# Kernel optimization log

Measured on AMD Instinct MI355X. Metric: run time of the kernel, lower is better.

## Reference

```python
import jax, jax.numpy as jnp
import numpy as np

HIDDEN = 2048
N_HEADS = 16
HEAD_DIM = HIDDEN // N_HEADS
MAX_POS = 4096
ROPE_THETA = 10000.0
B, S = 2, 4096


def rotate_half(x):
    d = x.shape[-1] // 2
    return jnp.concatenate([-x[..., d:], x[..., :d]], axis=-1)


def make_rope_cache(seq_len, dim, base):
    inv_freq = 1.0 / (base ** (np.arange(0, dim, 2, dtype=np.float32) / dim))
    t = np.arange(seq_len, dtype=np.float32)
    freqs = np.einsum('i,j->ij', t, inv_freq)
    emb = np.concatenate([freqs, freqs], axis=-1)
    return jnp.asarray(np.cos(emb)), jnp.asarray(np.sin(emb))


def setup_inputs() -> dict:
    key = jax.random.key(0)
    k1, k2, k3, k4, k5, k6 = jax.random.split(key, 6)
    hidden_states = jax.random.normal(k1, (B, S, HIDDEN), dtype=jnp.float32)
    # causal additive mask [B,1,S,S]
    causal = jnp.where(jnp.tril(jnp.ones((S, S), dtype=bool)), 0.0, -1e9).astype(jnp.float32)
    attention_mask = jnp.broadcast_to(causal[None, None], (B, 1, S, S))
    position_ids = jnp.broadcast_to(jnp.arange(S, dtype=jnp.int64)[None], (B, S))
    scale = 0.02
    Wq = jax.random.normal(k2, (HIDDEN, HIDDEN), dtype=jnp.float32) * scale
    Wk = jax.random.normal(k3, (HIDDEN, HIDDEN), dtype=jnp.float32) * scale
    Wv = jax.random.normal(k4, (HIDDEN, HIDDEN), dtype=jnp.float32) * scale
    Wo = jax.random.normal(k5, (HIDDEN, HIDDEN), dtype=jnp.float32) * scale
    return {"hidden_states": hidden_states, "attention_mask": attention_mask,
            "position_ids": position_ids, "Wq": Wq, "Wk": Wk, "Wv": Wv, "Wo": Wo}


def reference(hidden_states, attention_mask, position_ids, Wq, Wk, Wv, Wo):
    bsz, q_len, _ = hidden_states.shape
    # projections (torch Linear: x @ W.T; here W stored as [in,out] -> x @ W)
    q = (hidden_states @ Wq).reshape(bsz, q_len, N_HEADS, HEAD_DIM).transpose(0, 2, 1, 3)
    k = (hidden_states @ Wk).reshape(bsz, q_len, N_HEADS, HEAD_DIM).transpose(0, 2, 1, 3)
    v = (hidden_states @ Wv).reshape(bsz, q_len, N_HEADS, HEAD_DIM).transpose(0, 2, 1, 3)
    cos_c, sin_c = make_rope_cache(q_len, HEAD_DIM, ROPE_THETA)
    cos = cos_c[position_ids][:, None]  # [B,1,S,Dh]
    sin = sin_c[position_ids][:, None]
    q = q * cos + rotate_half(q) * sin
    k = k * cos + rotate_half(k) * sin
    scores = jnp.einsum('bhqd,bhkd->bhqk', q, k) / jnp.sqrt(jnp.float32(HEAD_DIM))
    scores = scores + attention_mask
    probs = jax.nn.softmax(scores.astype(jnp.float32), axis=-1).astype(q.dtype)
    attn = jnp.einsum('bhqk,bhkd->bhqd', probs, v)
    attn = attn.transpose(0, 2, 1, 3).reshape(bsz, q_len, HIDDEN)
    return attn @ Wo
```

## Files before the change

kernel.cpp:

```cpp
#include <hip/hip_runtime.h>

#define HID 2048
#define NHEADS 16
#define DHEAD 128
#define BB 2
#define SS 4096
#define MTOT (BB * SS)

typedef __attribute__((ext_vector_type(8))) short short8;
typedef __attribute__((ext_vector_type(8))) unsigned short ushort8;
typedef __attribute__((ext_vector_type(4))) float floatx4;
typedef __attribute__((ext_vector_type(16))) float floatx16;

static __device__ __forceinline__ ushort f2bf(float f) {
  unsigned x = __float_as_uint(f);
  return (ushort)((x + 0x7fffu + ((x >> 16) & 1u)) >> 16);
}
static __device__ __forceinline__ float bf2f(ushort u) {
  return __uint_as_float(((unsigned)u) << 16);
}
static __device__ __forceinline__ unsigned cvtpk_bf16(float lo, float hi) {
  unsigned r;
  asm("v_cvt_pk_bf16_f32 %0, %1, %2" : "=v"(r) : "v"(lo), "v"(hi));
  return r;
}
static __device__ __forceinline__ void pl32swap(unsigned& a, unsigned& b) {
  asm volatile("v_permlane32_swap_b32 %0, %1" : "+v"(a), "+v"(b));
}
static __device__ __forceinline__ float exp2_fast(float x) {
  float r;
  asm("v_exp_f32 %0, %1" : "=v"(r) : "v"(x));
  return r;
}
static __device__ __forceinline__ floatx16 fz16() {
  floatx16 z;
#pragma unroll
  for (int i = 0; i < 16; i++) z[i] = 0.f;
  return z;
}

#define GL16(g, l)                                                   \
  __builtin_amdgcn_global_load_lds(                                  \
      (const __attribute__((address_space(1))) unsigned int*)(g),    \
      (__attribute__((address_space(3))) unsigned int*)(l), 16, 0, 0)

__global__ __launch_bounds__(256) void k_prep(const float* __restrict__ X,
                                              ushort* __restrict__ Xb,
                                              const float* __restrict__ Wq,
                                              const float* __restrict__ Wk,
                                              const float* __restrict__ Wv,
                                              const float* __restrict__ Wo,
                                              ushort* __restrict__ Wqt,
                                              ushort* __restrict__ Wkt,
                                              ushort* __restrict__ Wvt,
                                              ushort* __restrict__ Wot,
                                              float* __restrict__ cosT,
                                              float* __restrict__ sinT) {
  __shared__ float tile[64][65];
  int id = blockIdx.x, t = threadIdx.x;
  if (id < 2048) {
    int i = id * 256 + t;
    const int n4 = MTOT * HID / 4, stride = 2048 * 256;
    for (; i < n4; i += stride) {
      float4 v = reinterpret_cast<const float4*>(X)[i];
      ushort4 u;
      u.x = f2bf(v.x); u.y = f2bf(v.y); u.z = f2bf(v.z); u.w = f2bf(v.w);
      reinterpret_cast<ushort4*>(Xb)[i] = u;
    }
  } else if (id < 6144) {
    int w = (id - 2048) >> 10;
    int bid = (id - 2048) & 1023;
    const float* W = (w == 0) ? Wq : (w == 1) ? Wk : (w == 2) ? Wv : Wo;
    ushort* Wt = (w == 0) ? Wqt : (w == 1) ? Wkt : (w == 2) ? Wvt : Wot;
    int n0 = (bid & 31) * 64, k0 = (bid >> 5) * 64;
#pragma unroll
    for (int i = 0; i < 16; i++) {
      int idx = t + i * 256, r = idx >> 6, c = idx & 63;
      tile[r][c] = W[(size_t)(k0 + r) * HID + n0 + c];
    }
    __syncthreads();
#pragma unroll
    for (int i = 0; i < 16; i++) {
      int idx = t + i * 256, r = idx >> 6, c = idx & 63;
      Wt[(size_t)(n0 + r) * HID + k0 + c] = f2bf(tile[c][r]);
    }
  } else {
    int idx = (id - 6144) * 256 + t;
    int pos = idx >> 6, j = idx & 63;
    float inv = powf(10000.0f, -(float)(2 * j) * (1.0f / 128.0f));
    float a = (float)pos * inv;
    cosT[idx] = cosf(a);
    sinT[idx] = sinf(a);
  }
}

__global__ __launch_bounds__(512) void k_rope(ushort* __restrict__ Q,
                                              ushort* __restrict__ Kb,
                                              const float* __restrict__ cosT,
                                              const float* __restrict__ sinT) {
  const float kSc = 0.12751742f;
  int idx = blockIdx.x * 512 + threadIdx.x;
  int j8 = (idx & 7) * 8;
  int hh = (idx >> 3) & (NHEADS - 1);
  int srow = idx >> 7;
  int pos = srow & (SS - 1);
  float4 c0 = *reinterpret_cast<const float4*>(&cosT[pos * 64 + j8]);
  float4 c1 = *reinterpret_cast<const float4*>(&cosT[pos * 64 + j8 + 4]);
  float4 s0 = *reinterpret_cast<const float4*>(&sinT[pos * 64 + j8]);
  float4 s1 = *reinterpret_cast<const float4*>(&sinT[pos * 64 + j8 + 4]);
  float cc[8] = {c0.x, c0.y, c0.z, c0.w, c1.x, c1.y, c1.z, c1.w};
  float ss[8] = {s0.x, s0.y, s0.z, s0.w, s1.x, s1.y, s1.z, s1.w};
  size_t base = (size_t)srow * HID + hh * DHEAD + j8;
  ushort8 qa = *reinterpret_cast<ushort8*>(&Q[base]);
  ushort8 qb = *reinterpret_cast<ushort8*>(&Q[base + 64]);
  ushort8 ka = *reinterpret_cast<ushort8*>(&Kb[base]);
  ushort8 kb = *reinterpret_cast<ushort8*>(&Kb[base + 64]);
  ushort8 o1, o2, o3, o4;
#pragma unroll
  for (int i = 0; i < 8; i++) {
    float a1 = bf2f(qa[i]), a2 = bf2f(qb[i]);
    o1[i] = f2bf((a1 * cc[i] - a2 * ss[i]) * kSc);
    o2[i] = f2bf((a2 * cc[i] + a1 * ss[i]) * kSc);
    float b1 = bf2f(ka[i]), b2 = bf2f(kb[i]);
    o3[i] = f2bf(b1 * cc[i] - b2 * ss[i]);
    o4[i] = f2bf(b2 * cc[i] + b1 * ss[i]);
  }
  *reinterpret_cast<ushort8*>(&Q[base]) = o1;
  *reinterpret_cast<ushort8*>(&Q[base + 64]) = o2;
  *reinterpret_cast<ushort8*>(&Kb[base]) = o3;
  *reinterpret_cast<ushort8*>(&Kb[base + 64]) = o4;
}

template <int OUT_BF16, int TRIPLE>
__global__ __launch_bounds__(512, 2) void k_gemm8(const ushort* __restrict__ A,
                                                  const ushort* __restrict__ Bt,
                                                  void* __restrict__ Cp,
                                                  const ushort* __restrict__ Bt2,
                                                  void* __restrict__ Cp2,
                                                  const ushort* __restrict__ A3,
                                                  const ushort* __restrict__ Bt3,
                                                  void* __restrict__ Cp3,
                                                  int Nc0, int Kd) {
  __shared__ ushort As[3][256 * 32];
  __shared__ ushort Bs[3][256 * 32];
  int t = threadIdx.x;
  int lane = t & 63, wid = t >> 6;
  int lrow = lane & 15, lk = lane >> 4;
  int wr = wid >> 2, wc = wid & 3;

  int id = blockIdx.x;
  int Nc = Nc0;
  if (TRIPLE && id >= 512) {
    A = A3; Bt = Bt3; Cp = Cp3; Nc = MTOT;
    id -= 512;
  } else if (TRIPLE && id >= 256) {
    Bt = Bt2; Cp = Cp2;
    id -= 256;
  }
  int nbx = Nc >> 8;
  int swz = (id & 7) * 32 + (id >> 3);
  int m0 = (swz / nbx) << 8, n0 = (swz % nbx) << 8;

  floatx4 acc[8][4];
#pragma unroll
  for (int i = 0; i < 8; i++)
#pragma unroll
    for (int j = 0; j < 4; j++) acc[i][j] = (floatx4){0.f, 0.f, 0.f, 0.f};

  int arow = t >> 2;
  int acol = (((t & 3) ^ (arow & 3)) << 3);
  const ushort* gA = A + (size_t)(m0 + arow) * Kd + acol;
  const ushort* gB = Bt + (size_t)(n0 + arow) * Kd + acol;

  auto STAGE = [&](int buf, int kt) {
    const ushort* a = gA + kt * 32;
    const ushort* bq = gB + kt * 32;
    GL16(a, (char*)As + buf * 16384 + t * 16);
    GL16(a + (size_t)128 * Kd, (char*)As + buf * 16384 + t * 16 + 8192);
    GL16(bq, (char*)Bs + buf * 16384 + t * 16);
    GL16(bq + (size_t)128 * Kd, (char*)Bs + buf * 16384 + t * 16 + 8192);
  };

  STAGE(0, 0);
  STAGE(1, 1);

  int nk = Kd >> 5;
  for (int tK = 0; tK < nk; ++tK) {
    if (tK + 1 < nk)
      asm volatile("s_waitcnt vmcnt(4)" ::: "memory");
    else
      asm volatile("s_waitcnt vmcnt(0)" ::: "memory");
    __builtin_amdgcn_s_barrier();
    asm volatile("" ::: "memory");
    int buf = tK % 3;
    const char* Ab_ = (const char*)As + buf * 16384;
    const char* Bb_ = (const char*)Bs + buf * 16384;
    short8 af[8], bfr[4];
#pragma unroll
    for (int fm = 0; fm < 8; fm++) {
      int row = wr * 128 + fm * 16 + lrow;
      af[fm] = *reinterpret_cast<const short8*>(
          Ab_ + ((row * 64 + lk * 16) ^ ((row & 3) << 4)));
    }
#pragma unroll
    for (int fn = 0; fn < 4; fn++) {
      int row = wc * 64 + fn * 16 + lrow;
      bfr[fn] = *reinterpret_cast<const short8*>(
          Bb_ + ((row * 64 + lk * 16) ^ ((row & 3) << 4)));
    }
    if (tK + 2 < nk) STAGE((tK + 2) % 3, tK + 2);
    __builtin_amdgcn_s_setprio(1);
#pragma unroll
    for (int fm = 0; fm < 8; fm++)
#pragma unroll
      for (int fn = 0; fn < 4; fn++)
        acc[fm][fn] = __builtin_amdgcn_mfma_f32_16x16x32_bf16(af[fm], bfr[fn],
                                                              acc[fm][fn], 0, 0, 0);
    __builtin_amdgcn_s_setprio(0);
  }

#pragma unroll
  for (int am = 0; am < 8; am++)
#pragma unroll
    for (int an = 0; an < 4; an++)
#pragma unroll
      for (int r = 0; r < 4; r++) {
        int m = m0 + wr * 128 + am * 16 + lk * 4 + r;
        int n = n0 + wc * 64 + an * 16 + lrow;
        if (OUT_BF16)
          ((ushort*)Cp)[(size_t)m * Nc + n] = f2bf(acc[am][an][r]);
        else
          ((float*)Cp)[(size_t)m * Nc + n] = acc[am][an][r];
      }
}

__global__ __launch_bounds__(512, 2) void k_fattn(const ushort* __restrict__ Qg,
                                                  const ushort* __restrict__ Kg,
                                                  const ushort* __restrict__ Vt2,
                                                  ushort* __restrict__ Og) {
  __shared__ ushort Ks[2][64 * 128];
  __shared__ ushort Vs[2][128 * 64];
  int t = threadIdx.x, lane = t & 63, wid = t >> 6;
  int l31 = lane & 31, hi = lane >> 5;
  int id = blockIdx.x;
  int qt = 15 - (id >> 5);
  int h = id & 15, b = (id >> 4) & 1;

  auto STAGE = [&](int buf, int kt) {
    int kv0 = kt * 64;
    const ushort* Kbase = Kg + (size_t)(b * SS + kv0) * HID + h * DHEAD;
    const ushort* Vbase = Vt2 + (size_t)(h * DHEAD) * MTOT + b * SS + kv0;
#pragma unroll
    for (int i = 0; i < 2; i++) {
      int L = t + i * 512;
      int row = L >> 4, cr = L & 15;
      GL16(Kbase + (size_t)row * HID + ((cr ^ (row & 15)) << 3),
           (char*)Ks + buf * 16384 + L * 16);
    }
#pragma unroll
    for (int i = 0; i < 2; i++) {
      int L = t + i * 512;
      int row = L >> 3, cr = L & 7;
      GL16(Vbase + (size_t)row * MTOT + ((cr ^ (row & 7)) << 3),
           (char*)Vs + buf * 16384 + L * 16);
    }
  };

  int q0 = qt * 256;
  int wq0 = q0 + wid * 32;
  int qlane = wq0 + l31;

  short8 qf[8];
  {
    const ushort* qb = Qg + (size_t)(b * SS + qlane) * HID + h * DHEAD + hi * 8;
#pragma unroll
    for (int ks = 0; ks < 8; ks++)
      qf[ks] = *reinterpret_cast<const short8*>(qb + ks * 16);
  }

  floatx16 accO[4];
#pragma unroll
  for (int db = 0; db < 4; db++) accO[db] = fz16();
  float mrow = -1e30f, lsum = 0.f;

  int nkt = (qt + 1) * 4;
  STAGE(0, 0);

  for (int kt = 0; kt < nkt; kt++) {
    int cur = kt & 1;
    int kv0 = kt * 64;
    bool pre = (kt + 1 < nkt);
    if (pre) {
      STAGE(cur ^ 1, kt + 1);
      asm volatile("s_waitcnt vmcnt(4)" ::: "memory");
    } else {
      asm volatile("s_waitcnt vmcnt(0)" ::: "memory");
    }
    __builtin_amdgcn_s_barrier();
    asm volatile("" ::: "memory");

    if (kv0 <= wq0 + 31) {
      const char* Kb_ = (const char*)Ks + cur * 16384;
      floatx16 accS[2];
      accS[0] = fz16(); accS[1] = fz16();
      __builtin_amdgcn_s_setprio(1);
#pragma unroll
      for (int ks = 0; ks < 8; ks++) {
#pragma unroll
        for (int kvb = 0; kvb < 2; kvb++) {
          int row = kvb * 32 + l31;
          int byte_ = (row * 256 + ks * 32 + hi * 16) ^ ((row & 15) << 4);
          short8 kf = *reinterpret_cast<const short8*>(Kb_ + byte_);
          accS[kvb] = __builtin_amdgcn_mfma_f32_32x32x16_bf16(kf, qf[ks], accS[kvb], 0, 0, 0);
        }
      }
      __builtin_amdgcn_s_setprio(0);

      if (kv0 + 63 > wq0) {
        int kvbase = kv0 + hi * 4;
#pragma unroll
        for (int kvb = 0; kvb < 2; kvb++)
#pragma unroll
          for (int r = 0; r < 16; r++) {
            int kvi = kvbase + kvb * 32 + (r & 3) + 8 * (r >> 2);
            if (kvi > qlane) accS[kvb][r] = -1e30f;
          }
      }

      float mA = -1e30f, mB = -1e30f, mC = -1e30f, mD = -1e30f;
#pragma unroll
      for (int r = 0; r < 16; r += 4) {
        mA = fmaxf(mA, fmaxf(accS[0][r], accS[1][r]));
        mB = fmaxf(mB, fmaxf(accS[0][r + 1], accS[1][r + 1]));
        mC = fmaxf(mC, fmaxf(accS[0][r + 2], accS[1][r + 2]));
        mD = fmaxf(mD, fmaxf(accS[0][r + 3], accS[1][r + 3]));
      }
      float mx = fmaxf(fmaxf(mA, mB), fmaxf(mC, mD));
      mx = fmaxf(mx, __shfl_xor(mx, 32));
      if (!__all(mx <= mrow + 8.0f)) {
        float mnew = fmaxf(mrow, mx);
        float corr = exp2_fast(mrow - mnew);
        mrow = mnew;
        lsum *= corr;
#pragma unroll
        for (int db = 0; db < 4; db++)
#pragma unroll
          for (int r = 0; r < 16; r++) accO[db][r] *= corr;
      }

      float sA = 0.f, sB = 0.f, sC = 0.f, sD = 0.f;
#pragma unroll
      for (int kvb = 0; kvb < 2; kvb++)
#pragma unroll
        for (int r = 0; r < 16; r += 4) {
          float p0 = exp2_fast(accS[kvb][r] - mrow);
          float p1 = exp2_fast(accS[kvb][r + 1] - mrow);
          float p2 = exp2_fast(accS[kvb][r + 2] - mrow);
          float p3 = exp2_fast(accS[kvb][r + 3] - mrow);
          accS[kvb][r] = p0; accS[kvb][r + 1] = p1;
          accS[kvb][r + 2] = p2; accS[kvb][r + 3] = p3;
          sA += p0; sB += p1; sC += p2; sD += p3;
        }
      lsum += ((sA + sB) + (sC + sD));

      const char* Vb_ = (const char*)Vs + cur * 16384;
#pragma unroll
      for (int ks = 0; ks < 4; ks++) {
        int kvb = ks >> 1, tt = ks & 1;
        unsigned w0 = cvtpk_bf16(accS[kvb][8 * tt + 0], accS[kvb][8 * tt + 1]);
        unsigned w2 = cvtpk_bf16(accS[kvb][8 * tt + 4], accS[kvb][8 * tt + 5]);
        pl32swap(w0, w2);
        unsigned w1 = cvtpk_bf16(accS[kvb][8 * tt + 2], accS[kvb][8 * tt + 3]);
        unsigned w3 = cvtpk_bf16(accS[kvb][8 * tt + 6], accS[kvb][8 * tt + 7]);
        pl32swap(w1, w3);
        union { unsigned u[4]; short8 v; } pf;
        pf.u[0] = w0; pf.u[1] = w1; pf.u[2] = w2; pf.u[3] = w3;
        __builtin_amdgcn_s_setprio(1);
#pragma unroll
        for (int db = 0; db < 4; db++) {
          int row = db * 32 + l31;
          int byte_ = (row * 128 + ks * 32 + hi * 16) ^ ((row & 7) << 4);
          short8 vf = *reinterpret_cast<const short8*>(Vb_ + byte_);
          accO[db] = __builtin_amdgcn_mfma_f32_32x32x16_bf16(vf, pf.v, accO[db], 0, 0, 0);
        }
        __builtin_amdgcn_s_setprio(0);
      }
    }
    asm volatile("" ::: "memory");
    __builtin_amdgcn_s_barrier();
    asm volatile("" ::: "memory");
  }

  float lt = lsum + __shfl_xor(lsum, 32);
  float inv = 1.0f / lt;
  char* sb = ((wid < 4) ? (char*)Ks : (char*)Vs) + (wid & 3) * 8192;
#pragma unroll
  for (int db = 0; db < 4; db++)
#pragma unroll
    for (int r = 0; r < 16; r += 2) {
      int d = db * 32 + (r & 3) + 8 * (r >> 2) + hi * 4;
      unsigned w = cvtpk_bf16(accO[db][r] * inv, accO[db][r + 1] * inv);
      int byte_ = (l31 * 256 + d * 2) ^ ((l31 & 15) << 4);
      *reinterpret_cast<unsigned*>(sb + byte_) = w;
    }
#pragma unroll
  for (int i = 0; i < 8; i++) {
    int row = i * 4 + (lane >> 4);
    int byte_ = (row * 256 + (lane & 15) * 16) ^ ((row & 15) << 4);
    ushort8 ov = *reinterpret_cast<const ushort8*>(sb + byte_);
    *reinterpret_cast<ushort8*>(Og + (size_t)(b * SS + wq0 + row) * HID + h * DHEAD +
                                (lane & 15) * 8) = ov;
  }
}

extern "C" void kernel_launch(void* const* d_in, const int* in_sizes, int n_in,
                              void* d_out, int out_size, void* d_ws, size_t ws_size,
                              hipStream_t stream) {
  const float* X = (const float*)d_in[0];
  const float* Wq = (const float*)d_in[3];
  const float* Wk = (const float*)d_in[4];
  const float* Wv = (const float*)d_in[5];
  const float* Wo = (const float*)d_in[6];
  float* out = (float*)d_out;

  char* p = (char*)d_ws;
  const size_t szXb = (size_t)MTOT * HID * 2;
  const size_t szW = (size_t)HID * HID * 2;
  ushort* Xb = (ushort*)p;  p += szXb;
  ushort* Wqt = (ushort*)p; p += szW;
  ushort* Wkt = (ushort*)p; p += szW;
  ushort* Wvt = (ushort*)p; p += szW;
  ushort* Wot = (ushort*)p; p += szW;
  ushort* Qb = (ushort*)p;  p += szXb;
  ushort* Kb = (ushort*)p;  p += szXb;
  ushort* Vt2 = (ushort*)p; p += szXb;
  ushort* Ab = (ushort*)p;  p += szXb;
  float* cosT = (float*)p;  p += (size_t)SS * 64 * 4;
  float* sinT = (float*)p;  p += (size_t)SS * 64 * 4;

  k_prep<<<7168, 256, 0, stream>>>(X, Xb, Wq, Wk, Wv, Wo, Wqt, Wkt, Wvt, Wot,
                                   cosT, sinT);

  k_gemm8<1, 1><<<768, 512, 0, stream>>>(Xb, Wqt, Qb, Wkt, Kb, Wvt, Xb, Vt2,
                                         HID, HID);
  k_rope<<<MTOT * NHEADS * 8 / 512, 512, 0, stream>>>(Qb, Kb, cosT, sinT);

  k_fattn<<<512, 512, 0, stream>>>(Qb, Kb, Vt2, Ab);

  k_gemm8<0, 0><<<256, 512, 0, stream>>>(Ab, Wot, out, nullptr, nullptr,
                                         nullptr, nullptr, nullptr, HID, HID);
}
```

Baseline: 488.1 us.

## Split GEMM k-step into two half-phases interleaving LDS reads, staging, and MFMA

Each K iteration of the bf16 projection GEMM becomes two phases. Each phase reads half of the A fragments, issues half of the next-stage global loads (A then B), passes a barrier, and runs 16 MFMAs. The goal is to overlap LDS reads and global staging with MFMA work and to lower fragment register pressure, in the style of a ping-pong schedule. It adds an extra workgroup barrier per iteration and uses sched_barrier to pin instruction order, which may stall waves or interact poorly with the existing vmcnt(4) wait accounting.

Measured after the change: 505.0 us. 1.03x slower.

```diff
diff --git a/kernel.cpp b/kernel.cpp
--- a/kernel.cpp
+++ b/kernel.cpp
@@ -172,17 +172,19 @@
   const ushort* gA = A + (size_t)(m0 + arow) * Kd + acol;
   const ushort* gB = Bt + (size_t)(n0 + arow) * Kd + acol;
 
-  auto STAGE = [&](int buf, int kt) {
+  auto STAGE_A = [&](int buf, int kt) {
     const ushort* a = gA + kt * 32;
-    const ushort* bq = gB + kt * 32;
     GL16(a, (char*)As + buf * 16384 + t * 16);
     GL16(a + (size_t)128 * Kd, (char*)As + buf * 16384 + t * 16 + 8192);
+  };
+  auto STAGE_B = [&](int buf, int kt) {
+    const ushort* bq = gB + kt * 32;
     GL16(bq, (char*)Bs + buf * 16384 + t * 16);
     GL16(bq + (size_t)128 * Kd, (char*)Bs + buf * 16384 + t * 16 + 8192);
   };
 
-  STAGE(0, 0);
-  STAGE(1, 1);
+  STAGE_A(0, 0); STAGE_B(0, 0);
+  STAGE_A(1, 1); STAGE_B(1, 1);
 
   int nk = Kd >> 5;
   for (int tK = 0; tK < nk; ++tK) {
@@ -195,28 +197,52 @@
     int buf = tK % 3;
     const char* Ab_ = (const char*)As + buf * 16384;
     const char* Bb_ = (const char*)Bs + buf * 16384;
-    short8 af[8], bfr[4];
-#pragma unroll
-    for (int fm = 0; fm < 8; fm++) {
-      int row = wr * 128 + fm * 16 + lrow;
-      af[fm] = *reinterpret_cast<const short8*>(
-          Ab_ + ((row * 64 + lk * 16) ^ ((row & 3) << 4)));
-    }
+
+    short8 bfr[4], af0[4];
 #pragma unroll
     for (int fn = 0; fn < 4; fn++) {
       int row = wc * 64 + fn * 16 + lrow;
       bfr[fn] = *reinterpret_cast<const short8*>(
           Bb_ + ((row * 64 + lk * 16) ^ ((row & 3) << 4)));
     }
-    if (tK + 2 < nk) STAGE((tK + 2) % 3, tK + 2);
+#pragma unroll
+    for (int fm = 0; fm < 4; fm++) {
+      int row = wr * 128 + fm * 16 + lrow;
+      af0[fm] = *reinterpret_cast<const short8*>(
+          Ab_ + ((row * 64 + lk * 16) ^ ((row & 3) << 4)));
+    }
+    if (tK + 2 < nk) STAGE_A((tK + 2) % 3, tK + 2);
+    __builtin_amdgcn_sched_barrier(0);
+    __builtin_amdgcn_s_barrier();
     __builtin_amdgcn_s_setprio(1);
 #pragma unroll
-    for (int fm = 0; fm < 8; fm++)
+    for (int fm = 0; fm < 4; fm++)
 #pragma unroll
       for (int fn = 0; fn < 4; fn++)
-        acc[fm][fn] = __builtin_amdgcn_mfma_f32_16x16x32_bf16(af[fm], bfr[fn],
+        acc[fm][fn] = __builtin_amdgcn_mfma_f32_16x16x32_bf16(af0[fm], bfr[fn],
                                                               acc[fm][fn], 0, 0, 0);
     __builtin_amdgcn_s_setprio(0);
+    __builtin_amdgcn_sched_barrier(0);
+
+    short8 af1[4];
+#pragma unroll
+    for (int fm = 0; fm < 4; fm++) {
+      int row = wr * 128 + 64 + fm * 16 + lrow;
+      af1[fm] = *reinterpret_cast<const short8*>(
+          Ab_ + ((row * 64 + lk * 16) ^ ((row & 3) << 4)));
+    }
+    if (tK + 2 < nk) STAGE_B((tK + 2) % 3, tK + 2);
+    __builtin_amdgcn_sched_barrier(0);
+    __builtin_amdgcn_s_barrier();
+    __builtin_amdgcn_s_setprio(1);
+#pragma unroll
+    for (int fm = 0; fm < 4; fm++)
+#pragma unroll
+      for (int fn = 0; fn < 4; fn++)
+        acc[fm + 4][fn] = __builtin_amdgcn_mfma_f32_16x16x32_bf16(af1[fm], bfr[fn],
+                                                                  acc[fm + 4][fn], 0, 0, 0);
+    __builtin_amdgcn_s_setprio(0);
+    __builtin_amdgcn_sched_barrier(0);
   }
 
 #pragma unroll
```
